# Optimization experiments

Measured on AMD Instinct MI355X. Metric: run time of the kernel, lower is better.

## Reference

```python
import jax, jax.numpy as jnp
import numpy as np

N_NODES = 500_000
N_HYPER = 5_000_000
N_ADJ = 16_000_000


def setup_inputs() -> dict:
    key = jax.random.key(0)
    k1, k2, k3 = jax.random.split(key, 3)
    x = jax.random.uniform(k1, (N_NODES,), dtype=jnp.float32)
    hyper_edges = jax.random.randint(k2, (N_HYPER, 3), 0, N_NODES, dtype=jnp.int32)
    adj_edges = jax.random.randint(k3, (N_ADJ, 2), 0, N_NODES, dtype=jnp.int32)
    return {"x": x, "t": 0, "hyper_edges": hyper_edges, "adj_edges": adj_edges}


def reference(x, t, hyper_edges, adj_edges):
    # x: [N] node states; hyper_edges: [E,3] size-3 hyperedges; adj_edges: [M,2] (src,dst)
    N = x.shape[0]

    # --- hyperedge gather-product-scatter (update_result_3, vectorized) ---
    xe = x[hyper_edges]                       # [E,3] gathered member states
    prod = xe[:, 1] * xe[:, 2]                # product over nodes[1:]
    vals = prod[:, None] - xe * xe            # [E,3] per-member contribution
    hyper_res = jax.ops.segment_sum(
        vals.reshape(-1), hyper_edges.reshape(-1), num_segments=N)

    # --- sparse Laplacian SpMV: L@x = deg*x - A@x (edge-list form) ---
    src = adj_edges[:, 0]
    dst = adj_edges[:, 1]
    Ax = jax.ops.segment_sum(x[src], dst, num_segments=N)
    deg = jax.ops.segment_sum(jnp.ones_like(src, dtype=x.dtype), dst, num_segments=N)
    Lx = deg * x - Ax

    # forward: -0.1 * L@x + 0.9 * hyperedge result
    return -0.1 * Lx + 0.9 * hyper_res
```

## Files before the change

kernel.cpp:

```cpp
#include <hip/hip_runtime.h>
#include <hip/hip_fp16.h>


#define W_BUCKET   8192
#define W_SHIFT    13
#define NB_MAX     62
#define S_STAGE    128
#define A_THREADS  512
#define A_BLOCKS   1024
#define ADJ_TILE   4096
#define HYP_TILE   1536
#define B_PB       16
#define CAP_A      262144
#define CAP_H      245760
#define SRC_MASK   0x7FFFFu


__global__ __launch_bounds__(256) void zero_f4_kernel(float4* __restrict__ p, long long n4) {
    long long tid = (long long)blockIdx.x * blockDim.x + threadIdx.x;
    long long stride = (long long)gridDim.x * blockDim.x;
    for (long long i = tid; i < n4; i += stride) p[i] = make_float4(0.f, 0.f, 0.f, 0.f);
}

__global__ __launch_bounds__(256) void fused_scatter_kernel(
    const float* __restrict__ x, const int2* __restrict__ adj,
    const int* __restrict__ hyper, float* __restrict__ out,
    int n_adj, int n_hyper)
{
    const long long tid = (long long)blockIdx.x * blockDim.x + threadIdx.x;
    const long long stride = (long long)gridDim.x * blockDim.x;
    for (long long i = tid; i < n_adj; i += stride) {
        int2 e = adj[i];
        atomicAdd(&out[e.y], 0.1f * (x[e.x] - x[e.y]));
    }
    for (long long i = tid; i < n_hyper; i += stride) {
        int i0 = hyper[3*i], i1 = hyper[3*i+1], i2 = hyper[3*i+2];
        float x0 = x[i0], x1 = x[i1], x2 = x[i2];
        float p = x1 * x2;
        atomicAdd(&out[i0], 0.9f * (p - x0*x0));
        atomicAdd(&out[i1], 0.9f * (p - x1*x1));
        atomicAdd(&out[i2], 0.9f * (p - x2*x2));
    }
}


__global__ __launch_bounds__(256) void zero_int_kernel(int* __restrict__ p, int n) {
    int tid = blockIdx.x * blockDim.x + threadIdx.x;
    int stride = gridDim.x * blockDim.x;
    for (int i = tid; i < n; i += stride) p[i] = 0;
}


template <int KIND>
__device__ __forceinline__ void flush_stage(int nb, int* cur, int* basev, int* cnts,
                                            unsigned int* stage,
                                            int* __restrict__ g_cursor,
                                            unsigned int* __restrict__ g_records,
                                            long long cap,
                                            const float* __restrict__ x,
                                            float* __restrict__ g_direct,
                                            int wave, int lane, int nwaves) {
    __syncthreads();
    if (wave == 0 && lane < nb) {
        int c = min(cur[lane], S_STAGE);
        cur[lane] = 0;
        int base = 0;
        if (c > 0) base = atomicAdd(&g_cursor[lane], c);
        basev[lane] = base;
        cnts[lane]  = c;
    }
    __syncthreads();
    for (int b = wave; b < nb; b += nwaves) {
        int c = cnts[b];
        long long base = basev[b];
        for (int r = lane; r < c; r += 64) {
            long long idx = base + r;
            unsigned int rec = stage[b * S_STAGE + r];
            if (idx < cap) {
                g_records[(long long)b * cap + idx] = rec;
            } else if (KIND == 0) {
                int src = rec & SRC_MASK;
                int dst = b * W_BUCKET + (int)(rec >> 19);
                atomicAdd(&g_direct[dst], 0.1f * (x[src] - x[dst]));
            } else {
                float v = __half2float(__ushort_as_half((unsigned short)(rec & 0xffffu)));
                atomicAdd(&g_direct[b * W_BUCKET + (int)(rec >> 16)], v);
            }
        }
    }
    __syncthreads();
}

__global__ __launch_bounds__(A_THREADS) void binning_kernel(
    const float* __restrict__ x,
    const int*  __restrict__ adj_raw, int n_adj,
    const int*  __restrict__ hyper, int n_hyper,
    int* __restrict__ cur_a, int* __restrict__ cur_h,
    float* __restrict__ g_direct,
    unsigned int* __restrict__ rec_a,
    unsigned int* __restrict__ rec_h,
    int nb)
{
    __shared__ unsigned int stage[NB_MAX * S_STAGE];
    __shared__ int cur[NB_MAX];
    __shared__ int basev[NB_MAX];
    __shared__ int cnts[NB_MAX];

    const int tid = threadIdx.x;
    const int wave = tid >> 6;
    const int lane = tid & 63;
    const int nwaves = A_THREADS >> 6;

    for (int b = tid; b < nb; b += A_THREADS) cur[b] = 0;
    __syncthreads();

    {
        long long per_blk = ((n_adj + A_BLOCKS - 1) / A_BLOCKS + 7) & ~7LL;
        long long a0 = (long long)blockIdx.x * per_blk;
        long long a1 = min((long long)n_adj, a0 + per_blk);
        for (long long t0 = a0; t0 < a1; t0 += ADJ_TILE) {
            long long t1 = min(a1, t0 + ADJ_TILE);
            for (long long g = t0 + (long long)tid * 4; g < t1; g += (long long)A_THREADS * 4) {
                if (g + 4 <= t1) {
                    const int4* p4 = (const int4*)(adj_raw + 2 * g);
                    int4 ea = p4[0], eb = p4[1];
                    int s0 = ea.x, d0 = ea.y,  s1 = ea.z, d1 = ea.w;
                    int s2 = eb.x, d2 = eb.y,  s3 = eb.z, d3 = eb.w;
                    int b0 = d0 >> W_SHIFT, b1 = d1 >> W_SHIFT;
                    int b2 = d2 >> W_SHIFT, b3 = d3 >> W_SHIFT;
                    int p0 = atomicAdd(&cur[b0], 1);
                    int p1 = atomicAdd(&cur[b1], 1);
                    int p2 = atomicAdd(&cur[b2], 1);
                    int p3 = atomicAdd(&cur[b3], 1);
                    if (p0 < S_STAGE) stage[b0*S_STAGE+p0] = ((unsigned)(d0 & (W_BUCKET-1)) << 19) | (unsigned)s0;
                    else atomicAdd(&g_direct[d0], 0.1f * (x[s0] - x[d0]));
                    if (p1 < S_STAGE) stage[b1*S_STAGE+p1] = ((unsigned)(d1 & (W_BUCKET-1)) << 19) | (unsigned)s1;
                    else atomicAdd(&g_direct[d1], 0.1f * (x[s1] - x[d1]));
                    if (p2 < S_STAGE) stage[b2*S_STAGE+p2] = ((unsigned)(d2 & (W_BUCKET-1)) << 19) | (unsigned)s2;
                    else atomicAdd(&g_direct[d2], 0.1f * (x[s2] - x[d2]));
                    if (p3 < S_STAGE) stage[b3*S_STAGE+p3] = ((unsigned)(d3 & (W_BUCKET-1)) << 19) | (unsigned)s3;
                    else atomicAdd(&g_direct[d3], 0.1f * (x[s3] - x[d3]));
                } else {
                    for (long long i = g; i < t1; ++i) {
                        int s = adj_raw[2*i], d = adj_raw[2*i+1];
                        int b = d >> W_SHIFT;
                        int p = atomicAdd(&cur[b], 1);
                        if (p < S_STAGE) stage[b*S_STAGE+p] = ((unsigned)(d & (W_BUCKET-1)) << 19) | (unsigned)s;
                        else atomicAdd(&g_direct[d], 0.1f * (x[s] - x[d]));
                    }
                }
            }
            flush_stage<0>(nb, cur, basev, cnts, stage, cur_a, rec_a, CAP_A,
                           x, g_direct, wave, lane, nwaves);
        }
    }

    {
        long long per_blk = ((n_hyper + A_BLOCKS - 1) / A_BLOCKS + 7) & ~7LL;
        long long h0 = (long long)blockIdx.x * per_blk;
        long long h1 = min((long long)n_hyper, h0 + per_blk);
        for (long long t0 = h0; t0 < h1; t0 += HYP_TILE) {
            long long t1 = min(h1, t0 + HYP_TILE);
            for (long long g = t0 + (long long)tid * 4; g < t1; g += (long long)A_THREADS * 4) {
                if (g + 4 <= t1) {
                    const int4* p4 = (const int4*)(hyper + 3 * g);
                    int4 w0 = p4[0], w1 = p4[1], w2 = p4[2];
                    int idx[12] = { w0.x, w0.y, w0.z,  w0.w, w1.x, w1.y,
                                    w1.z, w1.w, w2.x,  w2.y, w2.z, w2.w };
                    float xv[12];
                    #pragma unroll
                    for (int k = 0; k < 12; ++k) xv[k] = x[idx[k]];
                    #pragma unroll
                    for (int e = 0; e < 4; ++e) {
                        float xa = xv[3*e], xb = xv[3*e+1], xc = xv[3*e+2];
                        float pr = xb * xc;
                        int ia = idx[3*e], ib = idx[3*e+1], ic = idx[3*e+2];
                        int ba = ia >> W_SHIFT, bb = ib >> W_SHIFT, bc = ic >> W_SHIFT;
                        int pa = atomicAdd(&cur[ba], 1);
                        int pb = atomicAdd(&cur[bb], 1);
                        int pc = atomicAdd(&cur[bc], 1);
                        float va = 0.9f * (pr - xa*xa);
                        float vb = 0.9f * (pr - xb*xb);
                        float vc = 0.9f * (pr - xc*xc);
                        if (pa < S_STAGE) stage[ba*S_STAGE+pa] = ((unsigned)(ia & (W_BUCKET-1)) << 16) | (unsigned)__half_as_ushort(__float2half(va));
                        else atomicAdd(&g_direct[ia], va);
                        if (pb < S_STAGE) stage[bb*S_STAGE+pb] = ((unsigned)(ib & (W_BUCKET-1)) << 16) | (unsigned)__half_as_ushort(__float2half(vb));
                        else atomicAdd(&g_direct[ib], vb);
                        if (pc < S_STAGE) stage[bc*S_STAGE+pc] = ((unsigned)(ic & (W_BUCKET-1)) << 16) | (unsigned)__half_as_ushort(__float2half(vc));
                        else atomicAdd(&g_direct[ic], vc);
                    }
                } else {
                    for (long long i = g; i < t1; ++i) {
                        int i0 = hyper[3*i], i1 = hyper[3*i+1], i2 = hyper[3*i+2];
                        float x0 = x[i0], x1 = x[i1], x2 = x[i2];
                        float pr = x1 * x2;
                        int b0 = i0 >> W_SHIFT, b1 = i1 >> W_SHIFT, b2 = i2 >> W_SHIFT;
                        int p0 = atomicAdd(&cur[b0], 1);
                        int p1 = atomicAdd(&cur[b1], 1);
                        int p2 = atomicAdd(&cur[b2], 1);
                        float v0 = 0.9f * (pr - x0*x0);
                        float v1 = 0.9f * (pr - x1*x1);
                        float v2 = 0.9f * (pr - x2*x2);
                        if (p0 < S_STAGE) stage[b0*S_STAGE+p0] = ((unsigned)(i0 & (W_BUCKET-1)) << 16) | (unsigned)__half_as_ushort(__float2half(v0));
                        else atomicAdd(&g_direct[i0], v0);
                        if (p1 < S_STAGE) stage[b1*S_STAGE+p1] = ((unsigned)(i1 & (W_BUCKET-1)) << 16) | (unsigned)__half_as_ushort(__float2half(v1));
                        else atomicAdd(&g_direct[i1], v1);
                        if (p2 < S_STAGE) stage[b2*S_STAGE+p2] = ((unsigned)(i2 & (W_BUCKET-1)) << 16) | (unsigned)__half_as_ushort(__float2half(v2));
                        else atomicAdd(&g_direct[i2], v2);
                    }
                }
            }
            flush_stage<1>(nb, cur, basev, cnts, stage, cur_h, rec_h, CAP_H,
                           x, g_direct, wave, lane, nwaves);
        }
    }
}


__global__ __launch_bounds__(512) void accumulate_kernel(
    const float* __restrict__ x,
    const unsigned int* __restrict__ rec_a,
    const unsigned int* __restrict__ rec_h,
    const int* __restrict__ cur_a,
    const int* __restrict__ cur_h,
    float* __restrict__ partials, int n_nodes)
{
    __shared__ float  acc[W_BUCKET];
    __shared__ __half xs[W_BUCKET];
    const int b = blockIdx.x / B_PB;
    const int j = blockIdx.x % B_PB;
    const int base_node = b * W_BUCKET;

    for (int i = threadIdx.x; i < W_BUCKET; i += 512) {
        acc[i] = 0.f;
        int n = base_node + i;
        xs[i] = __float2half(n < n_nodes ? x[n] : 0.f);
    }
    __syncthreads();

    {
        long long cnt = min(cur_a[b], CAP_A);
        long long g8 = (cnt + 7) >> 3;
        long long s8 = g8 * j / B_PB, e8 = g8 * (j + 1) / B_PB;
        const uint4* r4 = (const uint4*)(rec_a + (long long)b * CAP_A);
        for (long long i8 = s8 + threadIdx.x; i8 < e8; i8 += 512) {
            uint4 r0 = r4[2*i8], r1 = r4[2*i8 + 1];
            long long base = i8 << 3;
            unsigned rr[8] = { r0.x, r0.y, r0.z, r0.w, r1.x, r1.y, r1.z, r1.w };
            if (base + 7 < cnt) {
                float xv[8];
                #pragma unroll
                for (int k = 0; k < 8; ++k) xv[k] = x[rr[k] & SRC_MASK];
                #pragma unroll
                for (int k = 0; k < 8; ++k) {
                    int dl = rr[k] >> 19;
                    unsafeAtomicAdd(&acc[dl], 0.1f * (xv[k] - __half2float(xs[dl])));
                }
            } else {
                #pragma unroll
                for (int k = 0; k < 8; ++k) {
                    if (base + k < cnt) {
                        int dl = rr[k] >> 19;
                        unsafeAtomicAdd(&acc[dl],
                            0.1f * (x[rr[k] & SRC_MASK] - __half2float(xs[dl])));
                    }
                }
            }
        }
    }

    {
        long long cnt = min(cur_h[b], CAP_H);
        long long g8 = (cnt + 7) >> 3;
        long long s8 = g8 * j / B_PB, e8 = g8 * (j + 1) / B_PB;
        const uint4* r4 = (const uint4*)(rec_h + (long long)b * CAP_H);
        for (long long i8 = s8 + threadIdx.x; i8 < e8; i8 += 512) {
            uint4 r0 = r4[2*i8], r1 = r4[2*i8 + 1];
            long long base = i8 << 3;
            unsigned rr[8] = { r0.x, r0.y, r0.z, r0.w, r1.x, r1.y, r1.z, r1.w };
            #pragma unroll
            for (int k = 0; k < 8; ++k) {
                if (base + k < cnt) {
                    float v = __half2float(__ushort_as_half((unsigned short)(rr[k] & 0xffffu)));
                    unsafeAtomicAdd(&acc[rr[k] >> 16], v);
                }
            }
        }
    }
    __syncthreads();

    float* p = partials + (long long)blockIdx.x * W_BUCKET;
    for (int i = threadIdx.x; i < W_BUCKET; i += 512) p[i] = acc[i];
}


__global__ __launch_bounds__(256) void finalize_kernel(
    const float* __restrict__ partials,
    const float* __restrict__ g_direct,
    float* __restrict__ out, int n_nodes)
{
    int tid = blockIdx.x * blockDim.x + threadIdx.x;
    int stride = gridDim.x * blockDim.x;
    for (int n = tid; n < n_nodes; n += stride) {
        int b = n >> W_SHIFT, l = n & (W_BUCKET - 1);
        float s = g_direct[n];
        const float* p = partials + ((long long)b * B_PB) * W_BUCKET + l;
        #pragma unroll
        for (int j = 0; j < B_PB; ++j) s += p[(long long)j * W_BUCKET];
        out[n] = s;
    }
}


extern "C" void kernel_launch(void* const* d_in, const int* in_sizes, int n_in,
                              void* d_out, int out_size, void* d_ws, size_t ws_size,
                              hipStream_t stream) {
    const float* x     = (const float*)d_in[0];
    const int*   hyper = (const int*)d_in[2];
    const int*   adj   = (const int*)d_in[3];
    float*       out   = (float*)d_out;

    const int n_nodes = in_sizes[0];
    const int n_hyper = in_sizes[2] / 3;
    const int n_adj   = in_sizes[3] / 2;
    const int nb      = (n_nodes + W_BUCKET - 1) / W_BUCKET;

    const size_t off_cur    = 0;
    const size_t off_direct = 512;
    size_t off_ra = off_direct + (size_t)n_nodes * 4;
    off_ra = (off_ra + 255) & ~(size_t)255;
    const size_t ra_bytes = (size_t)NB_MAX * CAP_A * 4;
    size_t off_rh = off_ra + ra_bytes;
    const size_t rh_bytes = (size_t)NB_MAX * CAP_H * 4;
    size_t off_part = off_rh + rh_bytes;
    off_part = (off_part + 255) & ~(size_t)255;
    const size_t part_bytes = (size_t)NB_MAX * B_PB * W_BUCKET * 4;
    const size_t need = off_part + part_bytes;

    if (nb <= NB_MAX && n_nodes <= (1 << 19) && (n_nodes & 3) == 0 && ws_size >= need) {
        int*          cur_a    = (int*)          ((char*)d_ws + off_cur);
        int*          cur_h    = (int*)          ((char*)d_ws + off_cur + 256);
        float*        g_direct = (float*)        ((char*)d_ws + off_direct);
        unsigned int* rec_a    = (unsigned int*) ((char*)d_ws + off_ra);
        unsigned int* rec_h    = (unsigned int*) ((char*)d_ws + off_rh);
        float*        partials = (float*)        ((char*)d_ws + off_part);

        zero_int_kernel<<<256, 256, 0, stream>>>((int*)d_ws, (int)(off_ra / 4));

        binning_kernel<<<A_BLOCKS, A_THREADS, 0, stream>>>(
            x, adj, n_adj, hyper, n_hyper, cur_a, cur_h, g_direct, rec_a, rec_h, nb);

        accumulate_kernel<<<nb * B_PB, 512, 0, stream>>>(
            x, rec_a, rec_h, cur_a, cur_h, partials, n_nodes);

        finalize_kernel<<<1024, 256, 0, stream>>>(partials, g_direct, out, n_nodes);
    } else {
        zero_f4_kernel<<<512, 256, 0, stream>>>((float4*)out, n_nodes / 4);
        fused_scatter_kernel<<<2048, 256, 0, stream>>>(x, (const int2*)adj, hyper, out,
                                                       n_adj, n_hyper);
    }
}
```

Before: 519.5 us.

## Use nontemporal vector loads/stores, prefetch records, retune tiles and flush sync

Several changes at once. Streaming edge and record reads and writes become nontemporal vector accesses, and the accumulate loops software-prefetch the next records. The finalize kernel is vectorized to float4 with a smaller grid. flush_stage drops one barrier by having each wave reserve its own bucket space through a lane-0 atomic and a shuffle, and tile sizes and launch bounds are retuned. These aim to cut cache pollution, latency stalls and synchronization overhead, at the cost of more register pressure and larger LDS staging bursts per flush.

```diff
diff --git a/kernel.cpp b/kernel.cpp
--- a/kernel.cpp
+++ b/kernel.cpp
@@ -8,12 +8,19 @@
 #define S_STAGE    128
 #define A_THREADS  512
 #define A_BLOCKS   1024
-#define ADJ_TILE   4096
-#define HYP_TILE   1536
+#define ADJ_TILE   6144
+#define HYP_TILE   2048
 #define B_PB       16
 #define CAP_A      262144
 #define CAP_H      245760
 #define SRC_MASK   0x7FFFFu
+
+typedef int      v4i __attribute__((ext_vector_type(4)));
+typedef unsigned v4u __attribute__((ext_vector_type(4)));
+typedef float    v4f __attribute__((ext_vector_type(4)));
+
+#define NT_LOAD(p)     __builtin_nontemporal_load(p)
+#define NT_STORE(v, p) __builtin_nontemporal_store((v), (p))
 
 
 __global__ __launch_bounds__(256) void zero_f4_kernel(float4* __restrict__ p, long long n4) {
@@ -52,7 +59,7 @@
 
 
 template <int KIND>
-__device__ __forceinline__ void flush_stage(int nb, int* cur, int* basev, int* cnts,
+__device__ __forceinline__ void flush_stage(int nb, int* cur,
                                             unsigned int* stage,
                                             int* __restrict__ g_cursor,
                                             unsigned int* __restrict__ g_records,
@@ -61,23 +68,20 @@
                                             float* __restrict__ g_direct,
                                             int wave, int lane, int nwaves) {
     __syncthreads();
-    if (wave == 0 && lane < nb) {
-        int c = min(cur[lane], S_STAGE);
-        cur[lane] = 0;
-        int base = 0;
-        if (c > 0) base = atomicAdd(&g_cursor[lane], c);
-        basev[lane] = base;
-        cnts[lane]  = c;
-    }
-    __syncthreads();
     for (int b = wave; b < nb; b += nwaves) {
-        int c = cnts[b];
-        long long base = basev[b];
+        int c = 0, base = 0;
+        if (lane == 0) {
+            c = min(cur[b], S_STAGE);
+            cur[b] = 0;
+            if (c > 0) base = atomicAdd(&g_cursor[b], c);
+        }
+        c    = __shfl(c, 0);
+        base = __shfl(base, 0);
         for (int r = lane; r < c; r += 64) {
-            long long idx = base + r;
+            long long idx = (long long)base + r;
             unsigned int rec = stage[b * S_STAGE + r];
             if (idx < cap) {
-                g_records[(long long)b * cap + idx] = rec;
+                NT_STORE(rec, &g_records[(long long)b * cap + idx]);
             } else if (KIND == 0) {
                 int src = rec & SRC_MASK;
                 int dst = b * W_BUCKET + (int)(rec >> 19);
@@ -91,7 +95,7 @@
     __syncthreads();
 }
 
-__global__ __launch_bounds__(A_THREADS) void binning_kernel(
+__global__ __launch_bounds__(A_THREADS, 8) void binning_kernel(
     const float* __restrict__ x,
     const int*  __restrict__ adj_raw, int n_adj,
     const int*  __restrict__ hyper, int n_hyper,
@@ -103,8 +107,6 @@
 {
     __shared__ unsigned int stage[NB_MAX * S_STAGE];
     __shared__ int cur[NB_MAX];
-    __shared__ int basev[NB_MAX];
-    __shared__ int cnts[NB_MAX];
 
     const int tid = threadIdx.x;
     const int wave = tid >> 6;
@@ -122,10 +124,11 @@
             long long t1 = min(a1, t0 + ADJ_TILE);
             for (long long g = t0 + (long long)tid * 4; g < t1; g += (long long)A_THREADS * 4) {
                 if (g + 4 <= t1) {
-                    const int4* p4 = (const int4*)(adj_raw + 2 * g);
-                    int4 ea = p4[0], eb = p4[1];
-                    int s0 = ea.x, d0 = ea.y,  s1 = ea.z, d1 = ea.w;
-                    int s2 = eb.x, d2 = eb.y,  s3 = eb.z, d3 = eb.w;
+                    const v4i* p4 = (const v4i*)(adj_raw + 2 * g);
+                    v4i ea = NT_LOAD(p4);
+                    v4i eb = NT_LOAD(p4 + 1);
+                    int s0 = ea[0], d0 = ea[1],  s1 = ea[2], d1 = ea[3];
+                    int s2 = eb[0], d2 = eb[1],  s3 = eb[2], d3 = eb[3];
                     int b0 = d0 >> W_SHIFT, b1 = d1 >> W_SHIFT;
                     int b2 = d2 >> W_SHIFT, b3 = d3 >> W_SHIFT;
                     int p0 = atomicAdd(&cur[b0], 1);
@@ -150,7 +153,7 @@
                     }
                 }
             }
-            flush_stage<0>(nb, cur, basev, cnts, stage, cur_a, rec_a, CAP_A,
+            flush_stage<0>(nb, cur, stage, cur_a, rec_a, CAP_A,
                            x, g_direct, wave, lane, nwaves);
         }
     }
@@ -163,10 +166,12 @@
             long long t1 = min(h1, t0 + HYP_TILE);
             for (long long g = t0 + (long long)tid * 4; g < t1; g += (long long)A_THREADS * 4) {
                 if (g + 4 <= t1) {
-                    const int4* p4 = (const int4*)(hyper + 3 * g);
-                    int4 w0 = p4[0], w1 = p4[1], w2 = p4[2];
-                    int idx[12] = { w0.x, w0.y, w0.z,  w0.w, w1.x, w1.y,
-                                    w1.z, w1.w, w2.x,  w2.y, w2.z, w2.w };
+                    const v4i* p4 = (const v4i*)(hyper + 3 * g);
+                    v4i w0 = NT_LOAD(p4);
+                    v4i w1 = NT_LOAD(p4 + 1);
+                    v4i w2 = NT_LOAD(p4 + 2);
+                    int idx[12] = { w0[0], w0[1], w0[2],  w0[3], w1[0], w1[1],
+                                    w1[2], w1[3], w2[0],  w2[1], w2[2], w2[3] };
                     float xv[12];
                     #pragma unroll
                     for (int k = 0; k < 12; ++k) xv[k] = x[idx[k]];
@@ -210,14 +215,14 @@
                     }
                 }
             }
-            flush_stage<1>(nb, cur, basev, cnts, stage, cur_h, rec_h, CAP_H,
+            flush_stage<1>(nb, cur, stage, cur_h, rec_h, CAP_H,
                            x, g_direct, wave, lane, nwaves);
         }
     }
 }
 
 
-__global__ __launch_bounds__(512) void accumulate_kernel(
+__global__ __launch_bounds__(512, 6) void accumulate_kernel(
     const float* __restrict__ x,
     const unsigned int* __restrict__ rec_a,
     const unsigned int* __restrict__ rec_h,
@@ -239,14 +244,19 @@
     __syncthreads();
 
     {
-        long long cnt = min(cur_a[b], CAP_A);
+        long long cnt = min((long long)cur_a[b], (long long)CAP_A);
         long long g8 = (cnt + 7) >> 3;
         long long s8 = g8 * j / B_PB, e8 = g8 * (j + 1) / B_PB;
-        const uint4* r4 = (const uint4*)(rec_a + (long long)b * CAP_A);
-        for (long long i8 = s8 + threadIdx.x; i8 < e8; i8 += 512) {
-            uint4 r0 = r4[2*i8], r1 = r4[2*i8 + 1];
+        const v4u* r4 = (const v4u*)(rec_a + (long long)b * CAP_A);
+        long long i8 = s8 + threadIdx.x;
+        v4u r0 = {0,0,0,0}, r1 = {0,0,0,0};
+        if (i8 < e8) { r0 = NT_LOAD(r4 + 2*i8); r1 = NT_LOAD(r4 + 2*i8 + 1); }
+        while (i8 < e8) {
+            long long nx = i8 + 512;
+            v4u n0 = {0,0,0,0}, n1 = {0,0,0,0};
+            if (nx < e8) { n0 = NT_LOAD(r4 + 2*nx); n1 = NT_LOAD(r4 + 2*nx + 1); }
             long long base = i8 << 3;
-            unsigned rr[8] = { r0.x, r0.y, r0.z, r0.w, r1.x, r1.y, r1.z, r1.w };
+            unsigned rr[8] = { r0[0], r0[1], r0[2], r0[3], r1[0], r1[1], r1[2], r1[3] };
             if (base + 7 < cnt) {
                 float xv[8];
                 #pragma unroll
@@ -266,18 +276,24 @@
                     }
                 }
             }
+            r0 = n0; r1 = n1; i8 = nx;
         }
     }
 
     {
-        long long cnt = min(cur_h[b], CAP_H);
+        long long cnt = min((long long)cur_h[b], (long long)CAP_H);
         long long g8 = (cnt + 7) >> 3;
         long long s8 = g8 * j / B_PB, e8 = g8 * (j + 1) / B_PB;
-        const uint4* r4 = (const uint4*)(rec_h + (long long)b * CAP_H);
-        for (long long i8 = s8 + threadIdx.x; i8 < e8; i8 += 512) {
-            uint4 r0 = r4[2*i8], r1 = r4[2*i8 + 1];
+        const v4u* r4 = (const v4u*)(rec_h + (long long)b * CAP_H);
+        long long i8 = s8 + threadIdx.x;
+        v4u r0 = {0,0,0,0}, r1 = {0,0,0,0};
+        if (i8 < e8) { r0 = NT_LOAD(r4 + 2*i8); r1 = NT_LOAD(r4 + 2*i8 + 1); }
+        while (i8 < e8) {
+            long long nx = i8 + 512;
+            v4u n0 = {0,0,0,0}, n1 = {0,0,0,0};
+            if (nx < e8) { n0 = NT_LOAD(r4 + 2*nx); n1 = NT_LOAD(r4 + 2*nx + 1); }
             long long base = i8 << 3;
-            unsigned rr[8] = { r0.x, r0.y, r0.z, r0.w, r1.x, r1.y, r1.z, r1.w };
+            unsigned rr[8] = { r0[0], r0[1], r0[2], r0[3], r1[0], r1[1], r1[2], r1[3] };
             #pragma unroll
             for (int k = 0; k < 8; ++k) {
                 if (base + k < cnt) {
@@ -285,12 +301,16 @@
                     unsafeAtomicAdd(&acc[rr[k] >> 16], v);
                 }
             }
+            r0 = n0; r1 = n1; i8 = nx;
         }
     }
     __syncthreads();
 
     float* p = partials + (long long)blockIdx.x * W_BUCKET;
-    for (int i = threadIdx.x; i < W_BUCKET; i += 512) p[i] = acc[i];
+    for (int i = threadIdx.x * 4; i < W_BUCKET; i += 512 * 4) {
+        v4f v = { acc[i], acc[i+1], acc[i+2], acc[i+3] };
+        NT_STORE(v, (v4f*)(p + i));
+    }
 }
 
 
@@ -301,13 +321,18 @@
 {
     int tid = blockIdx.x * blockDim.x + threadIdx.x;
     int stride = gridDim.x * blockDim.x;
-    for (int n = tid; n < n_nodes; n += stride) {
+    int n4 = n_nodes >> 2;
+    for (int q = tid; q < n4; q += stride) {
+        int n = q << 2;
         int b = n >> W_SHIFT, l = n & (W_BUCKET - 1);
-        float s = g_direct[n];
-        const float* p = partials + ((long long)b * B_PB) * W_BUCKET + l;
+        const float* pB = partials + ((long long)b * B_PB) * W_BUCKET + l;
+        v4f s = NT_LOAD((const v4f*)(g_direct + n));
         #pragma unroll
-        for (int j = 0; j < B_PB; ++j) s += p[(long long)j * W_BUCKET];
-        out[n] = s;
+        for (int jj = 0; jj < B_PB; ++jj) {
+            v4f pv = NT_LOAD((const v4f*)(pB + (long long)jj * W_BUCKET));
+            s += pv;
+        }
+        *(v4f*)(out + n) = s;
     }
 }
 
@@ -353,7 +378,7 @@
         accumulate_kernel<<<nb * B_PB, 512, 0, stream>>>(
             x, rec_a, rec_h, cur_a, cur_h, partials, n_nodes);
 
-        finalize_kernel<<<1024, 256, 0, stream>>>(partials, g_direct, out, n_nodes);
+        finalize_kernel<<<512, 256, 0, stream>>>(partials, g_direct, out, n_nodes);
     } else {
         zero_f4_kernel<<<512, 256, 0, stream>>>((float4*)out, n_nodes / 4);
         fused_scatter_kernel<<<2048, 256, 0, stream>>>(x, (const int2*)adj, hyper, out,
```

Measured after the change: 2.076 ms. 300% more time.
